# Kernel optimization log

Measured on AMD Instinct MI355X. Metric: run time of the kernel, lower is better.

## Reference

```python
import jax, jax.numpy as jnp
import numpy as np

B, V, H, T, D, HD = 4, 384, 128, 16, 8, 64
N = V + H  # 512
relu = jax.nn.relu


def setup_inputs() -> dict:
    key = jax.random.key(0)
    ks = jax.random.split(key, 12)

    def w(k, i, o):
        return (jax.random.normal(k, (i, o), jnp.float32) / np.sqrt(i)).astype(jnp.float32)

    return {
        "x": jax.random.normal(ks[0], (B, V, T, D), jnp.float32),
        "adj": jax.random.uniform(ks[1], (B, N, N), jnp.float32),
        # input_proj: Linear(T*D, HD) -> ReLU -> Linear(HD, HD) -> ReLU
        "w_in1": w(ks[2], T * D, HD), "b_in1": jnp.zeros((HD,), jnp.float32),
        "w_in2": w(ks[3], HD, HD), "b_in2": jnp.zeros((HD,), jnp.float32),
        # edge_mlp: Linear(2*HD, HD) -> ReLU -> Linear(HD, HD) -> ReLU
        "w_e1": w(ks[4], 2 * HD, HD), "b_e1": jnp.zeros((HD,), jnp.float32),
        "w_e2": w(ks[5], HD, HD), "b_e2": jnp.zeros((HD,), jnp.float32),
        # node_mlp: Linear(HD, HD) -> ReLU -> Linear(HD, HD) -> ReLU
        "w_n1": w(ks[6], HD, HD), "b_n1": jnp.zeros((HD,), jnp.float32),
        "w_n2": w(ks[7], HD, HD), "b_n2": jnp.zeros((HD,), jnp.float32),
        # out_proj: Linear(HD, T*D)
        "w_out": w(ks[8], HD, T * D), "b_out": jnp.zeros((T * D,), jnp.float32),
    }


def reference(x, adj, w_in1, b_in1, w_in2, b_in2, w_e1, b_e1, w_e2, b_e2,
              w_n1, b_n1, w_n2, b_n2, w_out, b_out):
    # node embedding of visible nodes: (B,V,HD)
    h = relu(relu(x.reshape(B, V, T * D) @ w_in1 + b_in1) @ w_in2 + b_in2)
    # pad hidden nodes with zeros: (B,N,HD)
    h_full = jnp.zeros((B, N, HD), x.dtype).at[:, :V].set(h)
    # edge_mlp layer 1 on cat([h_i, h_j]): split weight instead of materializing
    # the (B,N,N,2*HD) concatenation — same math.
    a = h_full @ w_e1[:HD]   # receiver-side contribution (B,N,HD)
    b = h_full @ w_e1[HD:]   # sender-side contribution  (B,N,HD)
    e = relu(a[:, :, None, :] + b[:, None, :, :] + b_e1)   # (B,N,N,HD)
    e = relu(e @ w_e2 + b_e2)                               # (B,N,N,HD)
    # mask by adjacency and sum over senders j
    agg = jnp.einsum('bijh,bij->bih', e, adj)               # (B,N,HD)
    n = relu(relu(agg @ w_n1 + b_n1) @ w_n2 + b_n2)         # (B,N,HD)
    out = n[:, V:] @ w_out + b_out                          # (B,H,T*D)
    return out.reshape(B, H, T, D)
```

## Files before the change

### kernel.cpp

```cpp
#include <hip/hip_runtime.h>

#define BQ 4
#define VV 384
#define HH 128
#define NN 512
#define HDIM 64
#define TD 128

__device__ __forceinline__ float BCAST(float v, int l) {
    return __int_as_float(__builtin_amdgcn_readlane(__float_as_int(v), l));
}

__global__ __launch_bounds__(256) void k_rowpipe(
    const float* __restrict__ x,
    const float* __restrict__ w_in1,
    const float* __restrict__ b_in1,
    const float* __restrict__ w_in2,
    const float* __restrict__ b_in2,
    const float* __restrict__ w_e1,
    const float* __restrict__ b_e1,
    const float* __restrict__ w_e2,
    const float* __restrict__ b_e2,
    float* __restrict__ E2)
{
    __shared__ float part[4][2][2][HDIM];

    const int wid  = threadIdx.x >> 6;
    const int lane = threadIdx.x & 63;
    const int rl   = wid >> 1;
    const int hf   = wid & 1;
    const int row  = blockIdx.x * 2 + rl;

    const float* xr = x + (size_t)row * TD;
    const float xv = xr[64 * hf + lane];

    float a0 = 0.f, a1 = 0.f;
    #pragma unroll 8
    for (int k = 0; k < 64; k += 2) {
        const int kg = 64 * hf + k;
        a0 = fmaf(BCAST(xv, k),     w_in1[kg * HDIM + lane],       a0);
        a1 = fmaf(BCAST(xv, k + 1), w_in1[(kg + 1) * HDIM + lane], a1);
    }
    part[0][rl][hf][lane] = a0 + a1;
    __syncthreads();
    const float h1 = fmaxf(part[0][rl][0][lane] + part[0][rl][1][lane] + b_in1[lane], 0.f);

    a0 = 0.f; a1 = 0.f;
    #pragma unroll 8
    for (int k = 0; k < 32; k += 2) {
        const int kg = 32 * hf + k;
        a0 = fmaf(BCAST(h1, kg),     w_in2[kg * HDIM + lane],       a0);
        a1 = fmaf(BCAST(h1, kg + 1), w_in2[(kg + 1) * HDIM + lane], a1);
    }
    part[1][rl][hf][lane] = a0 + a1;
    __syncthreads();
    const float h2 = fmaxf(part[1][rl][0][lane] + part[1][rl][1][lane] + b_in2[lane], 0.f);

    a0 = 0.f; a1 = 0.f;
    #pragma unroll 8
    for (int k = 0; k < 32; k += 2) {
        const int kg = 32 * hf + k;
        a0 = fmaf(BCAST(h2, kg),     w_e1[(HDIM + kg) * HDIM + lane],     a0);
        a1 = fmaf(BCAST(h2, kg + 1), w_e1[(HDIM + kg + 1) * HDIM + lane], a1);
    }
    part[2][rl][hf][lane] = a0 + a1;
    __syncthreads();
    const float e1 = fmaxf(part[2][rl][0][lane] + part[2][rl][1][lane] + b_e1[lane], 0.f);

    a0 = 0.f; a1 = 0.f;
    #pragma unroll 8
    for (int k = 0; k < 32; k += 2) {
        const int kg = 32 * hf + k;
        a0 = fmaf(BCAST(e1, kg),     w_e2[kg * HDIM + lane],       a0);
        a1 = fmaf(BCAST(e1, kg + 1), w_e2[(kg + 1) * HDIM + lane], a1);
    }
    part[3][rl][hf][lane] = a0 + a1;
    __syncthreads();
    if (hf == 0)
        E2[(size_t)row * HDIM + lane] =
            fmaxf(part[3][rl][0][lane] + part[3][rl][1][lane] + b_e2[lane], 0.f);
}

__global__ __launch_bounds__(1024) void k_agg_out(
    const float* __restrict__ adj,
    const float* __restrict__ E2,
    const float* __restrict__ b_e1, const float* __restrict__ w_e2,
    const float* __restrict__ b_e2,
    const float* __restrict__ w_n1, const float* __restrict__ b_n1,
    const float* __restrict__ w_n2, const float* __restrict__ b_n2,
    const float* __restrict__ w_out,
    const float* __restrict__ b_out,
    float* __restrict__ out)
{
    const int blk  = blockIdx.x;
    const int b    = blk >> 6;
    const int pair = blk & 63;
    const int wid  = threadIdx.x >> 6;
    const int lane = threadIdx.x & 63;

    const int i0 = VV + pair * 2;
    const float* adjr0 = adj + ((size_t)b * NN + i0) * NN;
    const float* adjr1 = adjr0 + NN;
    const int j0 = wid * 32;

    const float adjv = (lane < 32) ? adjr0[j0 + lane] : adjr1[j0 + lane - 32];

    __shared__ float redA[12][2][HDIM];
    __shared__ float hs[4][2];
    __shared__ float e2c[HDIM];

    if (wid < 12) {
        const float* e2b = E2 + ((size_t)b * VV + j0) * HDIM;
        float p0 = 0.f, p1 = 0.f, q0 = 0.f, q1 = 0.f;
        #pragma unroll 8
        for (int jj = 0; jj < 32; jj += 2) {
            const float e0 = e2b[jj * HDIM + lane];
            const float e1 = e2b[(jj + 1) * HDIM + lane];
            p0 = fmaf(BCAST(adjv, jj),      e0, p0);
            q0 = fmaf(BCAST(adjv, 32 + jj), e0, q0);
            p1 = fmaf(BCAST(adjv, jj + 1),  e1, p1);
            q1 = fmaf(BCAST(adjv, 33 + jj), e1, q1);
        }
        redA[wid][0][lane] = p0 + p1;
        redA[wid][1][lane] = q0 + q1;
    } else {
        float s = adjv;
        s += __shfl_xor(s, 1, 64);
        s += __shfl_xor(s, 2, 64);
        s += __shfl_xor(s, 4, 64);
        s += __shfl_xor(s, 8, 64);
        s += __shfl_xor(s, 16, 64);
        if (lane == 0)  hs[wid - 12][0] = s;
        if (lane == 32) hs[wid - 12][1] = s;
        if (wid == 12) {
            const float e1c = fmaxf(b_e1[lane], 0.f);
            float t0 = b_e2[lane], t1 = 0.f;
            #pragma unroll 8
            for (int k = 0; k < HDIM; k += 2) {
                t0 = fmaf(BCAST(e1c, k),     w_e2[k * HDIM + lane],       t0);
                t1 = fmaf(BCAST(e1c, k + 1), w_e2[(k + 1) * HDIM + lane], t1);
            }
            e2c[lane] = fmaxf(t0 + t1, 0.f);
        }
    }
    __syncthreads();

    const int g  = wid >> 3;
    const int w8 = wid & 7;

    const float hsum = hs[0][g] + hs[1][g] + hs[2][g] + hs[3][g];
    float agg = hsum * e2c[lane];
    #pragma unroll
    for (int w = 0; w < 12; ++w) agg += redA[w][g][lane];

    __shared__ float redB[16][HDIM];
    {
        float t0 = 0.f, t1 = 0.f;
        #pragma unroll
        for (int t = 0; t < 8; t += 2) {
            const int k = 8 * w8 + t;
            t0 = fmaf(BCAST(agg, k),     w_n1[k * HDIM + lane],       t0);
            t1 = fmaf(BCAST(agg, k + 1), w_n1[(k + 1) * HDIM + lane], t1);
        }
        redB[wid][lane] = t0 + t1;
    }
    __syncthreads();
    float n1 = b_n1[lane];
    #pragma unroll
    for (int w = 0; w < 8; ++w) n1 += redB[g * 8 + w][lane];
    n1 = fmaxf(n1, 0.f);

    __shared__ float redC[16][HDIM];
    {
        float t0 = 0.f, t1 = 0.f;
        #pragma unroll
        for (int t = 0; t < 8; t += 2) {
            const int k = 8 * w8 + t;
            t0 = fmaf(BCAST(n1, k),     w_n2[k * HDIM + lane],       t0);
            t1 = fmaf(BCAST(n1, k + 1), w_n2[(k + 1) * HDIM + lane], t1);
        }
        redC[wid][lane] = t0 + t1;
    }
    __syncthreads();
    float n2 = b_n2[lane];
    #pragma unroll
    for (int w = 0; w < 8; ++w) n2 += redC[g * 8 + w][lane];
    n2 = fmaxf(n2, 0.f);

    __shared__ float redD[16][TD];
    {
        float o0 = 0.f, o1 = 0.f;
        #pragma unroll
        for (int t = 0; t < 8; ++t) {
            const int k = 8 * w8 + t;
            const float v = BCAST(n2, k);
            o0 = fmaf(v, w_out[k * TD + lane],      o0);
            o1 = fmaf(v, w_out[k * TD + 64 + lane], o1);
        }
        redD[wid][lane]      = o0;
        redD[wid][64 + lane] = o1;
    }
    __syncthreads();

    if (w8 < 2) {
        const int col = w8 * 64 + lane;
        float o = b_out[col];
        #pragma unroll
        for (int w = 0; w < 8; ++w) o += redD[g * 8 + w][col];
        const int orow = b * HH + pair * 2 + g;
        out[(size_t)orow * TD + col] = o;
    }
}

extern "C" void kernel_launch(void* const* d_in, const int* in_sizes, int n_in,
                              void* d_out, int out_size, void* d_ws, size_t ws_size,
                              hipStream_t stream) {
    const float* x     = (const float*)d_in[0];
    const float* adj   = (const float*)d_in[1];
    const float* w_in1 = (const float*)d_in[2];
    const float* b_in1 = (const float*)d_in[3];
    const float* w_in2 = (const float*)d_in[4];
    const float* b_in2 = (const float*)d_in[5];
    const float* w_e1  = (const float*)d_in[6];
    const float* b_e1  = (const float*)d_in[7];
    const float* w_e2  = (const float*)d_in[8];
    const float* b_e2  = (const float*)d_in[9];
    const float* w_n1  = (const float*)d_in[10];
    const float* b_n1  = (const float*)d_in[11];
    const float* w_n2  = (const float*)d_in[12];
    const float* b_n2  = (const float*)d_in[13];
    const float* w_out = (const float*)d_in[14];
    const float* b_out = (const float*)d_in[15];
    float* out = (float*)d_out;
    float* E2  = (float*)d_ws;

    k_rowpipe<<<(BQ * VV) / 2, 256, 0, stream>>>(
        x, w_in1, b_in1, w_in2, b_in2, w_e1, b_e1, w_e2, b_e2, E2);
    k_agg_out<<<BQ * HH / 2, 1024, 0, stream>>>(
        adj, E2, b_e1, w_e2, b_e2, w_n1, b_n1, w_n2, b_n2, w_out, b_out, out);
}
```

Baseline: 18.28 us.

## Use single-wave per row MLP chains, removing split-K shared-memory reductions

The row pipeline kernel now runs one 64-lane wave per row and computes each full 64-wide layer in registers. This replaces two waves per row that split K and reduced partial sums through shared memory with a barrier after every layer. The aggregation kernel's node MLP and output projection are likewise done by two waves per group with the full K loop, instead of eight-way split-K with three shared-memory reduction stages and barriers. The change removes barriers and LDS traffic but gives each wave a longer serial FMA chain, and most waves of the second kernel sit idle after the aggregation.

```diff
diff --git a/kernel.cpp b/kernel.cpp
--- a/kernel.cpp
+++ b/kernel.cpp
@@ -11,7 +11,7 @@
     return __int_as_float(__builtin_amdgcn_readlane(__float_as_int(v), l));
 }
 
-__global__ __launch_bounds__(256) void k_rowpipe(
+__global__ __launch_bounds__(64) void k_rowpipe(
     const float* __restrict__ x,
     const float* __restrict__ w_in1,
     const float* __restrict__ b_in1,
@@ -23,62 +23,44 @@
     const float* __restrict__ b_e2,
     float* __restrict__ E2)
 {
-    __shared__ float part[4][2][2][HDIM];
-
-    const int wid  = threadIdx.x >> 6;
-    const int lane = threadIdx.x & 63;
-    const int rl   = wid >> 1;
-    const int hf   = wid & 1;
-    const int row  = blockIdx.x * 2 + rl;
+    const int row  = blockIdx.x;
+    const int lane = threadIdx.x;
 
     const float* xr = x + (size_t)row * TD;
-    const float xv = xr[64 * hf + lane];
+    const float xv0 = xr[lane];
+    const float xv1 = xr[64 + lane];
 
-    float a0 = 0.f, a1 = 0.f;
+    float a0 = b_in1[lane], a1 = 0.f;
     #pragma unroll 8
-    for (int k = 0; k < 64; k += 2) {
-        const int kg = 64 * hf + k;
-        a0 = fmaf(BCAST(xv, k),     w_in1[kg * HDIM + lane],       a0);
-        a1 = fmaf(BCAST(xv, k + 1), w_in1[(kg + 1) * HDIM + lane], a1);
+    for (int k = 0; k < HDIM; ++k) {
+        a0 = fmaf(BCAST(xv0, k), w_in1[k * HDIM + lane],          a0);
+        a1 = fmaf(BCAST(xv1, k), w_in1[(HDIM + k) * HDIM + lane], a1);
     }
-    part[0][rl][hf][lane] = a0 + a1;
-    __syncthreads();
-    const float h1 = fmaxf(part[0][rl][0][lane] + part[0][rl][1][lane] + b_in1[lane], 0.f);
+    const float h1 = fmaxf(a0 + a1, 0.f);
+
+    a0 = b_in2[lane]; a1 = 0.f;
+    #pragma unroll 8
+    for (int k = 0; k < HDIM; k += 2) {
+        a0 = fmaf(BCAST(h1, k),     w_in2[k * HDIM + lane],       a0);
+        a1 = fmaf(BCAST(h1, k + 1), w_in2[(k + 1) * HDIM + lane], a1);
+    }
+    const float h2 = fmaxf(a0 + a1, 0.f);
 
     a0 = 0.f; a1 = 0.f;
     #pragma unroll 8
-    for (int k = 0; k < 32; k += 2) {
-        const int kg = 32 * hf + k;
-        a0 = fmaf(BCAST(h1, kg),     w_in2[kg * HDIM + lane],       a0);
-        a1 = fmaf(BCAST(h1, kg + 1), w_in2[(kg + 1) * HDIM + lane], a1);
+    for (int k = 0; k < HDIM; k += 2) {
+        a0 = fmaf(BCAST(h2, k),     w_e1[(HDIM + k) * HDIM + lane],     a0);
+        a1 = fmaf(BCAST(h2, k + 1), w_e1[(HDIM + k + 1) * HDIM + lane], a1);
     }
-    part[1][rl][hf][lane] = a0 + a1;
-    __syncthreads();
-    const float h2 = fmaxf(part[1][rl][0][lane] + part[1][rl][1][lane] + b_in2[lane], 0.f);
+    const float e1 = fmaxf(a0 + a1 + b_e1[lane], 0.f);
 
-    a0 = 0.f; a1 = 0.f;
+    a0 = b_e2[lane]; a1 = 0.f;
     #pragma unroll 8
-    for (int k = 0; k < 32; k += 2) {
-        const int kg = 32 * hf + k;
-        a0 = fmaf(BCAST(h2, kg),     w_e1[(HDIM + kg) * HDIM + lane],     a0);
-        a1 = fmaf(BCAST(h2, kg + 1), w_e1[(HDIM + kg + 1) * HDIM + lane], a1);
+    for (int k = 0; k < HDIM; k += 2) {
+        a0 = fmaf(BCAST(e1, k),     w_e2[k * HDIM + lane],       a0);
+        a1 = fmaf(BCAST(e1, k + 1), w_e2[(k + 1) * HDIM + lane], a1);
     }
-    part[2][rl][hf][lane] = a0 + a1;
-    __syncthreads();
-    const float e1 = fmaxf(part[2][rl][0][lane] + part[2][rl][1][lane] + b_e1[lane], 0.f);
-
-    a0 = 0.f; a1 = 0.f;
-    #pragma unroll 8
-    for (int k = 0; k < 32; k += 2) {
-        const int kg = 32 * hf + k;
-        a0 = fmaf(BCAST(e1, kg),     w_e2[kg * HDIM + lane],       a0);
-        a1 = fmaf(BCAST(e1, kg + 1), w_e2[(kg + 1) * HDIM + lane], a1);
-    }
-    part[3][rl][hf][lane] = a0 + a1;
-    __syncthreads();
-    if (hf == 0)
-        E2[(size_t)row * HDIM + lane] =
-            fmaxf(part[3][rl][0][lane] + part[3][rl][1][lane] + b_e2[lane], 0.f);
+    E2[(size_t)row * HDIM + lane] = fmaxf(a0 + a1, 0.f);
 }
 
 __global__ __launch_bounds__(1024) void k_agg_out(
@@ -147,69 +129,38 @@
 
     const int g  = wid >> 3;
     const int w8 = wid & 7;
+    if (w8 >= 2) return;
 
     const float hsum = hs[0][g] + hs[1][g] + hs[2][g] + hs[3][g];
     float agg = hsum * e2c[lane];
     #pragma unroll
     for (int w = 0; w < 12; ++w) agg += redA[w][g][lane];
 
-    __shared__ float redB[16][HDIM];
-    {
-        float t0 = 0.f, t1 = 0.f;
-        #pragma unroll
-        for (int t = 0; t < 8; t += 2) {
-            const int k = 8 * w8 + t;
-            t0 = fmaf(BCAST(agg, k),     w_n1[k * HDIM + lane],       t0);
-            t1 = fmaf(BCAST(agg, k + 1), w_n1[(k + 1) * HDIM + lane], t1);
-        }
-        redB[wid][lane] = t0 + t1;
+    float t0 = b_n1[lane], t1 = 0.f;
+    #pragma unroll 8
+    for (int k = 0; k < HDIM; k += 2) {
+        t0 = fmaf(BCAST(agg, k),     w_n1[k * HDIM + lane],       t0);
+        t1 = fmaf(BCAST(agg, k + 1), w_n1[(k + 1) * HDIM + lane], t1);
     }
-    __syncthreads();
-    float n1 = b_n1[lane];
-    #pragma unroll
-    for (int w = 0; w < 8; ++w) n1 += redB[g * 8 + w][lane];
-    n1 = fmaxf(n1, 0.f);
+    const float n1 = fmaxf(t0 + t1, 0.f);
 
-    __shared__ float redC[16][HDIM];
-    {
-        float t0 = 0.f, t1 = 0.f;
-        #pragma unroll
-        for (int t = 0; t < 8; t += 2) {
-            const int k = 8 * w8 + t;
-            t0 = fmaf(BCAST(n1, k),     w_n2[k * HDIM + lane],       t0);
-            t1 = fmaf(BCAST(n1, k + 1), w_n2[(k + 1) * HDIM + lane], t1);
-        }
-        redC[wid][lane] = t0 + t1;
+    t0 = b_n2[lane]; t1 = 0.f;
+    #pragma unroll 8
+    for (int k = 0; k < HDIM; k += 2) {
+        t0 = fmaf(BCAST(n1, k),     w_n2[k * HDIM + lane],       t0);
+        t1 = fmaf(BCAST(n1, k + 1), w_n2[(k + 1) * HDIM + lane], t1);
     }
-    __syncthreads();
-    float n2 = b_n2[lane];
-    #pragma unroll
-    for (int w = 0; w < 8; ++w) n2 += redC[g * 8 + w][lane];
-    n2 = fmaxf(n2, 0.f);
+    const float n2 = fmaxf(t0 + t1, 0.f);
 
-    __shared__ float redD[16][TD];
-    {
-        float o0 = 0.f, o1 = 0.f;
-        #pragma unroll
-        for (int t = 0; t < 8; ++t) {
-            const int k = 8 * w8 + t;
-            const float v = BCAST(n2, k);
-            o0 = fmaf(v, w_out[k * TD + lane],      o0);
-            o1 = fmaf(v, w_out[k * TD + 64 + lane], o1);
-        }
-        redD[wid][lane]      = o0;
-        redD[wid][64 + lane] = o1;
+    const int col = 64 * w8 + lane;
+    float o0 = b_out[col], o1 = 0.f;
+    #pragma unroll 8
+    for (int k = 0; k < HDIM; k += 2) {
+        o0 = fmaf(BCAST(n2, k),     w_out[k * TD + col],       o0);
+        o1 = fmaf(BCAST(n2, k + 1), w_out[(k + 1) * TD + col], o1);
     }
-    __syncthreads();
-
-    if (w8 < 2) {
-        const int col = w8 * 64 + lane;
-        float o = b_out[col];
-        #pragma unroll
-        for (int w = 0; w < 8; ++w) o += redD[g * 8 + w][col];
-        const int orow = b * HH + pair * 2 + g;
-        out[(size_t)orow * TD + col] = o;
-    }
+    const int orow = b * HH + pair * 2 + g;
+    out[(size_t)orow * TD + col] = o0 + o1;
 }
 
 extern "C" void kernel_launch(void* const* d_in, const int* in_sizes, int n_in,
@@ -234,7 +185,7 @@
     float* out = (float*)d_out;
     float* E2  = (float*)d_ws;
 
-    k_rowpipe<<<(BQ * VV) / 2, 256, 0, stream>>>(
+    k_rowpipe<<<BQ * VV, 64, 0, stream>>>(
         x, w_in1, b_in1, w_in2, b_in2, w_e1, b_e1, w_e2, b_e2, E2);
     k_agg_out<<<BQ * HH / 2, 1024, 0, stream>>>(
         adj, E2, b_e1, w_e2, b_e2, w_n1, b_n1, w_n2, b_n2, w_out, b_out, out);
```

New measurement: 19.14 us. +4.7%, slower.
